# Kernel optimization log

Measured on AMD Instinct MI355X. Metric: run time of the kernel, lower is better.

The kernel has to match this reference:

```python
import jax, jax.numpy as jnp
import numpy as np

N = 50000      # nodes
E = 400000     # edges (before self-loops)
IN = 128       # in_channels
OUT = 64       # out_channels (per-head; concat=False averages heads)
HEADS = 8      # heads of first GAT layer; second layer has 1 head
NEG_SLOPE = 0.2


def _glorot(key, shape, fan_in, fan_out):
    s = jnp.sqrt(2.0 / (fan_in + fan_out)).astype(jnp.float32)
    return jax.random.normal(key, shape, jnp.float32) * s


def setup_inputs() -> dict:
    key = jax.random.key(0)
    ks = jax.random.split(key, 10)
    x = jax.random.normal(ks[0], (N, IN), jnp.float32)
    edge_index = jax.random.randint(ks[1], (2, E), 0, N)
    # layer 1: heads=HEADS, per-head dim OUT
    W1 = _glorot(ks[2], (IN, HEADS * OUT), IN, HEADS * OUT)
    att_src1 = _glorot(ks[3], (HEADS, OUT), OUT, 1)
    att_dst1 = _glorot(ks[4], (HEADS, OUT), OUT, 1)
    b1 = jnp.zeros((OUT,), jnp.float32)
    # layer 2: heads=1
    W2 = _glorot(ks[5], (OUT, 1 * OUT), OUT, OUT)
    att_src2 = _glorot(ks[6], (1, OUT), OUT, 1)
    att_dst2 = _glorot(ks[7], (1, OUT), OUT, 1)
    b2 = jnp.zeros((OUT,), jnp.float32)
    return dict(x=x, edge_index=edge_index, W1=W1, att_src1=att_src1,
                att_dst1=att_dst1, b1=b1, W2=W2, att_src2=att_src2,
                att_dst2=att_dst2, b2=b2)


def gat_conv(x, edge_index, W, att_src, att_dst, bias, heads, ch):
    """PyG GATConv with concat=False (mean over heads), add_self_loops=True."""
    n = x.shape[0]
    loop = jnp.arange(n, dtype=edge_index.dtype)
    src = jnp.concatenate([edge_index[0], loop])  # [E+N]
    dst = jnp.concatenate([edge_index[1], loop])
    h = (x @ W).reshape(n, heads, ch)                     # [N, H, C]
    a_s = jnp.sum(h * att_src, axis=-1)                   # [N, H]
    a_d = jnp.sum(h * att_dst, axis=-1)                   # [N, H]
    e = jax.nn.leaky_relu(a_s[src] + a_d[dst], NEG_SLOPE)  # [E+N, H]
    # numerically stable segment softmax over incoming edges of each dst node
    emax = jax.lax.stop_gradient(
        jax.ops.segment_max(e, dst, num_segments=n))       # [N, H]
    ee = jnp.exp(e - emax[dst])
    denom = jax.ops.segment_sum(ee, dst, num_segments=n)  # [N, H]
    alpha = ee / denom[dst]                                # [E+N, H]
    out = jax.ops.segment_sum(alpha[:, :, None] * h[src], dst,
                              num_segments=n)              # [N, H, C]
    return out.mean(axis=1) + bias                         # [N, C]


def reference(x, edge_index, W1, att_src1, att_dst1, b1,
              W2, att_src2, att_dst2, b2):
    h = gat_conv(x, edge_index, W1, att_src1, att_dst1, b1, HEADS, OUT)
    h = jax.nn.elu(h)
    return gat_conv(h, edge_index, W2, att_src2, att_dst2, b2, 1, OUT)
```

## Files before the change

### kernel.cpp

```cpp
#include <hip/hip_runtime.h>
#include <cstdint>
#include <cstddef>

#define NEG_SLOPE 0.2f

typedef short bf16x8 __attribute__((ext_vector_type(8)));
typedef float f32x4 __attribute__((ext_vector_type(4)));
typedef float f32x2 __attribute__((ext_vector_type(2)));

__device__ __forceinline__ unsigned short f2bf(float f) {
  unsigned u = __float_as_uint(f);
  u = u + 0x7FFFu + ((u >> 16) & 1u);
  return (unsigned short)(u >> 16);
}
__device__ __forceinline__ float bf2f(unsigned short b) {
  return __uint_as_float((unsigned)b << 16);
}
__device__ __forceinline__ f32x2 unpk(unsigned xv) {
  f32x2 r;
  r.x = __uint_as_float(xv << 16);
  r.y = __uint_as_float(xv & 0xFFFF0000u);
  return r;
}
__device__ __forceinline__ float rlf(float v, int l) {
  return __uint_as_float(
      (unsigned)__builtin_amdgcn_readlane((int)__float_as_uint(v), l));
}

__global__ __launch_bounds__(256) void prep_all(
    const int* __restrict__ ei, int* __restrict__ counts,
    const float* __restrict__ x, unsigned short* __restrict__ xb,
    const float* __restrict__ W1, const float* __restrict__ att_s1,
    const float* __restrict__ att_d1, unsigned short* __restrict__ AsAdT,
    unsigned short* __restrict__ WbT,
    const float* __restrict__ W2, unsigned short* __restrict__ W2t,
    const float* __restrict__ att_s2, const float* __restrict__ att_d2,
    float* __restrict__ AsAd2,
    int E, int ET, int N, int B0, int B1) {
  int b = blockIdx.x, tid = threadIdx.x;
  if (b < B0) {
    int i = b * 256 + tid;
    if (i < ET) {
      int dst = (i < E) ? ei[E + i] : (i - E);
      atomicAdd(&counts[dst], 1);
    }
    return;
  }
  b -= B0;
  if (b < B1) {
    int i = b * 256 + tid;
    if (i < N * 32) {
      float4 v = ((const float4*)x)[i];
      ushort4 o;
      o.x = f2bf(v.x); o.y = f2bf(v.y); o.z = f2bf(v.z); o.w = f2bf(v.w);
      ((ushort4*)xb)[i] = o;
    }
    return;
  }
  b -= B1;
  if (b < 8) {
    int i = b * 256 + tid;
    int o = i >> 7, k = i & 127, h = o & 7;
    const float* att = (o < 8) ? att_s1 : att_d1;
    float s = 0.f;
    for (int c = 0; c < 64; c++) s += W1[(size_t)k * 512 + h * 64 + c] * att[h * 64 + c];
    AsAdT[i] = f2bf(s);
    return;
  }
  b -= 8;
  if (b < 256) {
    int i = b * 256 + tid;
    int o = i >> 10, k = i & 1023, h = k >> 7, c = k & 127;
    WbT[i] = f2bf(W1[(size_t)c * 512 + h * 64 + o]);
    return;
  }
  b -= 256;
  if (b < 16) {
    int i = b * 256 + tid;
    if (i < 64 * 64) {
      int k = i >> 6, nn = i & 63;
      W2t[(size_t)nn * 64 + k] = f2bf(W2[i]);
    }
    return;
  }
  {
    int i = tid;
    if (i < 128) {
      int o = i >> 6, k = i & 63;
      const float* att = (o == 0) ? att_s2 : att_d2;
      float s = 0.f;
      for (int c = 0; c < 64; c++) s += W2[(size_t)k * 64 + c] * att[c];
      AsAd2[i] = s;
    }
  }
}

__global__ __launch_bounds__(1024) void scan_dots(
    const int* __restrict__ counts, int* __restrict__ offsets,
    const unsigned short* __restrict__ xb, const unsigned short* __restrict__ AsAdT,
    float* __restrict__ asd, int n) {
  if (blockIdx.x == 0) {
    __shared__ int sums[1024];
    int t = threadIdx.x;
    int chunk = (n + 1023) >> 10;
    int start = t * chunk;
    int end = min(start + chunk, n);
    int s = 0;
    for (int i = start; i < end; i++) s += counts[i];
    sums[t] = s;
    __syncthreads();
    for (int off = 1; off < 1024; off <<= 1) {
      int v = (t >= off) ? sums[t - off] : 0;
      __syncthreads();
      sums[t] += v;
      __syncthreads();
    }
    int run = sums[t] - s;
    for (int i = start; i < end; i++) { offsets[i] = run; run += counts[i]; }
    if (t == 1023) offsets[n] = sums[1023];
    return;
  }
  int tid = threadIdx.x;
  int wave = tid >> 6, lane = tid & 63;
  int q = lane >> 4, t = lane & 15;
  int row0 = (blockIdx.x - 1) * 256 + wave * 16;
  int arow = row0 + t; if (arow > n - 1) arow = n - 1;
  const bf16x8* aptr = (const bf16x8*)(xb + (size_t)arow * 128);
  const bf16x8* bptr = (const bf16x8*)(AsAdT + t * 128);
  f32x4 acc = (f32x4){0.f, 0.f, 0.f, 0.f};
  #pragma unroll
  for (int s = 0; s < 4; s++)
    acc = __builtin_amdgcn_mfma_f32_16x16x32_bf16(aptr[s * 4 + q], bptr[s * 4 + q],
                                                  acc, 0, 0, 0);
  #pragma unroll
  for (int r = 0; r < 4; r++) {
    int row = row0 + q * 4 + r;
    if (row < n) asd[row * 16 + t] = acc[r];
  }
}

__global__ __launch_bounds__(256) void fill_csr(
    const int* __restrict__ ei, const int* __restrict__ offsets,
    int* __restrict__ cursor, int* __restrict__ srcs, int E, int ET) {
  int i = blockIdx.x * 256 + threadIdx.x;
  if (i >= ET) return;
  int src, dst;
  if (i < E) { src = ei[i]; dst = ei[E + i]; } else { src = dst = i - E; }
  int pos = atomicAdd(&cursor[dst], 1);
  srcs[offsets[dst] + pos] = src;
}

#define CONSUME8R(RV, W, ACC)                                         \
  _Pragma("unroll")                                                   \
  for (int k = 0; k < 8; k++) {                                       \
    f32x2 x2 = unpk(RV[k]);                                           \
    ACC[0] += x2 * rlf(W, k * 8 + 0);                                 \
    ACC[1] += x2 * rlf(W, k * 8 + 1);                                 \
    ACC[2] += x2 * rlf(W, k * 8 + 2);                                 \
    ACC[3] += x2 * rlf(W, k * 8 + 3);                                 \
    ACC[4] += x2 * rlf(W, k * 8 + 4);                                 \
    ACC[5] += x2 * rlf(W, k * 8 + 5);                                 \
    ACC[6] += x2 * rlf(W, k * 8 + 6);                                 \
    ACC[7] += x2 * rlf(W, k * 8 + 7);                                 \
  }

__global__ __launch_bounds__(1024, 8) void agg1_gemm(
    const int* __restrict__ offsets, const int* __restrict__ srcs,
    const float* __restrict__ asd, const unsigned short* __restrict__ xb,
    const unsigned short* __restrict__ WbT, const float* __restrict__ b1,
    const float* __restrict__ AsAd2, unsigned short* __restrict__ zb,
    float* __restrict__ as2, float* __restrict__ ad2, int N) {
  __shared__ unsigned short sh[16 * 1032];
  int tid = threadIdx.x;
  int wv = tid >> 6, lane = tid & 63;
  int nb = blockIdx.x;
  {
    int node = nb * 16 + wv;
    f32x2 acc[8];
    #pragma unroll
    for (int h = 0; h < 8; h++) acc[h] = (f32x2){0.f, 0.f};
    float wsl = 0.f;
    int beg = offsets[node], end = offsets[node + 1];
    int jl = end - 1;
    float adv = asd[(size_t)node * 16 + 8 + (lane & 7)];
    for (int cb = beg; cb < end; cb += 16) {
      int cnt = min(16, end - cb);
      int sAll = srcs[min(cb + (lane & 15), jl)];
      int swa = srcs[min(cb + (lane >> 3), jl)];
      float asva = asd[(size_t)swa * 16 + (lane & 7)];
      float asvb = 0.f;
      if (cnt > 8) {
        int swb = srcs[min(cb + 8 + (lane >> 3), jl)];
        asvb = asd[(size_t)swb * 16 + (lane & 7)];
      }
      unsigned rva[8], rvb[8];
      #pragma unroll
      for (int k = 0; k < 8; k++) {
        int se = __builtin_amdgcn_readlane(sAll, k);
        rva[k] = *(const unsigned*)&xb[(size_t)(unsigned)se * 128 + 2 * lane];
      }
      if (cnt > 8) {
        #pragma unroll
        for (int k = 0; k < 8; k++) {
          int se = __builtin_amdgcn_readlane(sAll, k + 8);
          rvb[k] = *(const unsigned*)&xb[(size_t)(unsigned)se * 128 + 2 * lane];
        }
      }
      float wa, wb = 0.f;
      {
        float v = asva + adv;
        v = (v > 0.f) ? v : NEG_SLOPE * v;
        wa = (cb + (lane >> 3) < end) ? __expf(v) : 0.f;
      }
      if (cnt > 8) {
        float v = asvb + adv;
        v = (v > 0.f) ? v : NEG_SLOPE * v;
        wb = (cb + 8 + (lane >> 3) < end) ? __expf(v) : 0.f;
      }
      wsl += wa + wb;
      CONSUME8R(rva, wa, acc);
      if (cnt > 8) { CONSUME8R(rvb, wb, acc); }
    }
    wsl += __shfl_xor(wsl, 8, 64);
    wsl += __shfl_xor(wsl, 16, 64);
    wsl += __shfl_xor(wsl, 32, 64);
    #pragma unroll
    for (int h = 0; h < 8; h++) {
      float tot = rlf(wsl, h);
      float iv = 0.125f / tot;
      unsigned o = (unsigned)f2bf(acc[h].x * iv) | ((unsigned)f2bf(acc[h].y * iv) << 16);
      *(unsigned*)&sh[wv * 1032 + h * 128 + 2 * lane] = o;
    }
  }
  __syncthreads();
  if (wv < 4) {
    int q = lane >> 4, t = lane & 15;
    f32x4 acc4 = (f32x4){0.f, 0.f, 0.f, 0.f};
    const unsigned short* bbase = WbT + (size_t)(wv * 16 + t) * 1024;
    #pragma unroll 8
    for (int s = 0; s < 32; s++) {
      bf16x8 af = *(const bf16x8*)&sh[t * 1032 + s * 32 + q * 8];
      bf16x8 bf = *(const bf16x8*)&bbase[s * 32 + q * 8];
      acc4 = __builtin_amdgcn_mfma_f32_16x16x32_bf16(af, bf, acc4, 0, 0, 0);
    }
    int col = wv * 16 + t;
    float bias = b1[col];
    float vs = AsAd2[col], vd = AsAd2[64 + col];
    #pragma unroll
    for (int r = 0; r < 4; r++) {
      int row = q * 4 + r;
      int node = nb * 16 + row;
      float v = acc4[r] + bias;
      v = (v > 0.f) ? v : (__expf(v) - 1.f);
      zb[(size_t)node * 64 + col] = f2bf(v);
      float s = v * vs, d = v * vd;
      #pragma unroll
      for (int off = 1; off < 16; off <<= 1) {
        s += __shfl_xor(s, off, 64);
        d += __shfl_xor(d, off, 64);
      }
      if (t == 0) {
        atomicAdd(&as2[node], s);
        atomicAdd(&ad2[node], d);
      }
    }
  }
}

__global__ __launch_bounds__(1024, 8) void agg2_gemm(
    const int* __restrict__ offsets, const int* __restrict__ srcs,
    const float* __restrict__ as2, const float* __restrict__ ad2,
    const unsigned short* __restrict__ zb, const unsigned short* __restrict__ W2t,
    const float* __restrict__ b2, float* __restrict__ out, int N) {
  __shared__ unsigned short sh[16 * 72];
  int tid = threadIdx.x;
  int wv = tid >> 6, lane = tid & 63;
  int nb = blockIdx.x;
  {
    int node = nb * 16 + wv;
    int half = lane >> 5;
    float adv = ad2[node];
    int beg = offsets[node], end = offsets[node + 1];
    int jl = end - 1;
    f32x2 acc = (f32x2){0.f, 0.f};
    float wsl = 0.f;
    for (int cb = beg; cb < end; cb += 16) {
      int cnt = min(16, end - cb);
      int sAll = srcs[min(cb + (lane & 15), jl)];
      float asv = as2[sAll];
      unsigned rv[8];
      #pragma unroll
      for (int k = 0; k < 4; k++) {
        int s0 = __builtin_amdgcn_readlane(sAll, 2 * k);
        int s1 = __builtin_amdgcn_readlane(sAll, 2 * k + 1);
        int se = half ? s1 : s0;
        rv[k] = *(const unsigned*)&zb[(size_t)(unsigned)se * 64 + 2 * (lane & 31)];
      }
      if (cnt > 8) {
        #pragma unroll
        for (int k = 4; k < 8; k++) {
          int s0 = __builtin_amdgcn_readlane(sAll, 2 * k);
          int s1 = __builtin_amdgcn_readlane(sAll, 2 * k + 1);
          int se = half ? s1 : s0;
          rv[k] = *(const unsigned*)&zb[(size_t)(unsigned)se * 64 + 2 * (lane & 31)];
        }
      }
      float v = asv + adv;
      v = (v > 0.f) ? v : NEG_SLOPE * v;
      float wl = (cb + (lane & 15) < end) ? __expf(v) : 0.f;
      if (lane < 16) wsl += wl;
      #pragma unroll
      for (int k = 0; k < 4; k++) {
        float w0 = rlf(wl, 2 * k);
        float w1 = rlf(wl, 2 * k + 1);
        float w = half ? w1 : w0;
        acc += unpk(rv[k]) * w;
      }
      if (cnt > 8) {
        #pragma unroll
        for (int k = 4; k < 8; k++) {
          float w0 = rlf(wl, 2 * k);
          float w1 = rlf(wl, 2 * k + 1);
          float w = half ? w1 : w0;
          acc += unpk(rv[k]) * w;
        }
      }
    }
    wsl += __shfl_xor(wsl, 1, 64);
    wsl += __shfl_xor(wsl, 2, 64);
    wsl += __shfl_xor(wsl, 4, 64);
    wsl += __shfl_xor(wsl, 8, 64);
    float tot = rlf(wsl, 0);
    acc.x += __shfl_xor(acc.x, 32, 64);
    acc.y += __shfl_xor(acc.y, 32, 64);
    if (lane < 32) {
      float inv = 1.f / tot;
      unsigned o = (unsigned)f2bf(acc.x * inv) | ((unsigned)f2bf(acc.y * inv) << 16);
      *(unsigned*)&sh[wv * 72 + 2 * lane] = o;
    }
  }
  __syncthreads();
  if (wv < 4) {
    int q = lane >> 4, t = lane & 15;
    f32x4 acc4 = (f32x4){0.f, 0.f, 0.f, 0.f};
    const unsigned short* bbase = W2t + (size_t)(wv * 16 + t) * 64;
    #pragma unroll
    for (int s = 0; s < 2; s++) {
      bf16x8 af = *(const bf16x8*)&sh[t * 72 + s * 32 + q * 8];
      bf16x8 bf = *(const bf16x8*)&bbase[s * 32 + q * 8];
      acc4 = __builtin_amdgcn_mfma_f32_16x16x32_bf16(af, bf, acc4, 0, 0, 0);
    }
    int col = wv * 16 + t;
    float bias = b2[col];
    #pragma unroll
    for (int r = 0; r < 4; r++) {
      int node = nb * 16 + q * 4 + r;
      if (node < N) out[(size_t)node * 64 + col] = acc4[r] + bias;
    }
  }
}

extern "C" void kernel_launch(void* const* d_in, const int* in_sizes, int n_in,
                              void* d_out, int out_size, void* d_ws, size_t ws_size,
                              hipStream_t stream) {
  const int IN = 128;
  const int N = in_sizes[0] / IN;
  const int E = in_sizes[1] / 2;
  const int ET = E + N;

  const float* x        = (const float*)d_in[0];
  const int*   ei       = (const int*)d_in[1];
  const float* W1       = (const float*)d_in[2];
  const float* att_src1 = (const float*)d_in[3];
  const float* att_dst1 = (const float*)d_in[4];
  const float* b1       = (const float*)d_in[5];
  const float* W2       = (const float*)d_in[6];
  const float* att_src2 = (const float*)d_in[7];
  const float* att_dst2 = (const float*)d_in[8];
  const float* b2       = (const float*)d_in[9];
  float* out = (float*)d_out;

  char* base = (char*)d_ws;
  size_t off = 0;
  auto alloc = [&](size_t bytes) -> char* {
    char* p = base + off;
    off = (off + bytes + 255) & ~(size_t)255;
    return p;
  };
  unsigned short* xb    = (unsigned short*)alloc((size_t)N * 128 * 2);
  unsigned short* AsAdT = (unsigned short*)alloc((size_t)16 * 128 * 2);
  unsigned short* WbT   = (unsigned short*)alloc((size_t)64 * 1024 * 2);
  unsigned short* W2t   = (unsigned short*)alloc((size_t)64 * 64 * 2);
  unsigned short* zb    = (unsigned short*)alloc((size_t)N * 64 * 2);
  float* AsAd2 = (float*)alloc((size_t)128 * 4);
  float* asd1  = (float*)alloc((size_t)N * 16 * 4);
  int* offsets = (int*)alloc((size_t)(N + 1) * 4);
  int* srcs    = (int*)alloc((size_t)ET * 4);
  char* zero_begin = base + off;
  int* counts  = (int*)alloc((size_t)N * 4);
  int* cursor  = (int*)alloc((size_t)N * 4);
  float* a_s2  = (float*)alloc((size_t)N * 4);
  float* a_d2  = (float*)alloc((size_t)N * 4);
  char* zero_end = base + off;

  hipMemsetAsync(zero_begin, 0, (size_t)(zero_end - zero_begin), stream);

  const int TB = 256;
  auto cdiv = [](int a, int b) { return (a + b - 1) / b; };

  int B0 = cdiv(ET, TB);
  int B1 = cdiv(N * 32, TB);
  prep_all<<<B0 + B1 + 8 + 256 + 16 + 1, TB, 0, stream>>>(
      ei, counts, x, xb, W1, att_src1, att_dst1, AsAdT, WbT, W2, W2t,
      att_src2, att_dst2, AsAd2, E, ET, N, B0, B1);

  scan_dots<<<1 + cdiv(N, 256), 1024, 0, stream>>>(counts, offsets, xb, AsAdT,
                                                   asd1, N);

  fill_csr<<<cdiv(ET, TB), TB, 0, stream>>>(ei, offsets, cursor, srcs, E, ET);

  agg1_gemm<<<cdiv(N, 16), 1024, 0, stream>>>(offsets, srcs, asd1, xb, WbT, b1,
                                              AsAd2, zb, a_s2, a_d2, N);

  agg2_gemm<<<cdiv(N, 16), 1024, 0, stream>>>(offsets, srcs, a_s2, a_d2, zb,
                                              W2t, b2, out, N);
}
```

Baseline: 320.1 us.

## Use MFMA for layer-1 per-head weighted neighbor aggregation

Replaces the scalar FMA-with-readlane accumulation in agg1_gemm with 16x16x32 bf16 MFMA ops. Each chunk of 32 edges now builds an attention-weight A fragment (heads x edges) and B fragments of gathered bf16 features, repacked via shuffles. The attention weights are quantized to bf16 and the per-head sums are taken over those quantized values so the normalization stays consistent. Occupancy hint is reduced to 4 waves per SIMD to fit the larger f32x4 accumulators, and half the MFMA output rows (heads 8-15) are wasted, which adds padding cost in exchange for matrix-core throughput.

```diff
diff --git a/kernel.cpp b/kernel.cpp
--- a/kernel.cpp
+++ b/kernel.cpp
@@ -7,6 +7,7 @@
 typedef short bf16x8 __attribute__((ext_vector_type(8)));
 typedef float f32x4 __attribute__((ext_vector_type(4)));
 typedef float f32x2 __attribute__((ext_vector_type(2)));
+typedef unsigned u32x4 __attribute__((ext_vector_type(4)));
 
 __device__ __forceinline__ unsigned short f2bf(float f) {
   unsigned u = __float_as_uint(f);
@@ -150,21 +151,7 @@
   srcs[offsets[dst] + pos] = src;
 }
 
-#define CONSUME8R(RV, W, ACC)                                         \
-  _Pragma("unroll")                                                   \
-  for (int k = 0; k < 8; k++) {                                       \
-    f32x2 x2 = unpk(RV[k]);                                           \
-    ACC[0] += x2 * rlf(W, k * 8 + 0);                                 \
-    ACC[1] += x2 * rlf(W, k * 8 + 1);                                 \
-    ACC[2] += x2 * rlf(W, k * 8 + 2);                                 \
-    ACC[3] += x2 * rlf(W, k * 8 + 3);                                 \
-    ACC[4] += x2 * rlf(W, k * 8 + 4);                                 \
-    ACC[5] += x2 * rlf(W, k * 8 + 5);                                 \
-    ACC[6] += x2 * rlf(W, k * 8 + 6);                                 \
-    ACC[7] += x2 * rlf(W, k * 8 + 7);                                 \
-  }
-
-__global__ __launch_bounds__(1024, 8) void agg1_gemm(
+__global__ __launch_bounds__(1024, 4) void agg1_gemm(
     const int* __restrict__ offsets, const int* __restrict__ srcs,
     const float* __restrict__ asd, const unsigned short* __restrict__ xb,
     const unsigned short* __restrict__ WbT, const float* __restrict__ b1,
@@ -176,60 +163,82 @@
   int nb = blockIdx.x;
   {
     int node = nb * 16 + wv;
-    f32x2 acc[8];
+    int g = lane >> 4;
+    int h8 = lane & 7;
+    f32x4 acc[8];
     #pragma unroll
-    for (int h = 0; h < 8; h++) acc[h] = (f32x2){0.f, 0.f};
-    float wsl = 0.f;
+    for (int c = 0; c < 8; c++) acc[c] = (f32x4){0.f, 0.f, 0.f, 0.f};
+    float dsum = 0.f;
     int beg = offsets[node], end = offsets[node + 1];
     int jl = end - 1;
-    float adv = asd[(size_t)node * 16 + 8 + (lane & 7)];
-    for (int cb = beg; cb < end; cb += 16) {
-      int cnt = min(16, end - cb);
-      int sAll = srcs[min(cb + (lane & 15), jl)];
-      int swa = srcs[min(cb + (lane >> 3), jl)];
-      float asva = asd[(size_t)swa * 16 + (lane & 7)];
-      float asvb = 0.f;
-      if (cnt > 8) {
-        int swb = srcs[min(cb + 8 + (lane >> 3), jl)];
-        asvb = asd[(size_t)swb * 16 + (lane & 7)];
-      }
-      unsigned rva[8], rvb[8];
-      #pragma unroll
-      for (int k = 0; k < 8; k++) {
-        int se = __builtin_amdgcn_readlane(sAll, k);
-        rva[k] = *(const unsigned*)&xb[(size_t)(unsigned)se * 128 + 2 * lane];
-      }
-      if (cnt > 8) {
+    float adv = asd[(size_t)node * 16 + 8 + h8];
+    unsigned s = (lane & 1) * 16;
+    unsigned s2 = 16 - s;
+    unsigned msk = 0xFFFFu << s;
+    int choff = lane & 14;
+    for (int cb = beg; cb < end; cb += 32) {
+      int sAll = srcs[min(cb + (lane & 31), jl)];
+      float wj[8];
+      float dloc = 0.f;
+      #pragma unroll
+      for (int j = 0; j < 8; j++) {
+        int e = g * 8 + j;
+        int se = __shfl(sAll, e, 64);
+        float asv = asd[(size_t)(unsigned)se * 16 + h8];
+        float v = asv + adv;
+        v = (v > 0.f) ? v : NEG_SLOPE * v;
+        float w = (cb + e < end) ? __expf(v) : 0.f;
+        float wq = bf2f(f2bf(w));
+        wj[j] = wq;
+        dloc += wq;
+      }
+      dloc += __shfl_xor(dloc, 16, 64);
+      dloc += __shfl_xor(dloc, 32, 64);
+      dsum += dloc;
+      u32x4 a4;
+      #pragma unroll
+      for (int d = 0; d < 4; d++)
+        a4[d] = (unsigned)f2bf(wj[2 * d]) | ((unsigned)f2bf(wj[2 * d + 1]) << 16);
+      bf16x8 afr = __builtin_bit_cast(bf16x8, a4);
+      int seh[4];
+      #pragma unroll
+      for (int hh = 0; hh < 4; hh++)
+        seh[hh] = __shfl(sAll, g * 8 + hh * 2 + (lane & 1), 64);
+      unsigned own[8][4];
+      #pragma unroll
+      for (int cg = 0; cg < 8; cg++) {
         #pragma unroll
-        for (int k = 0; k < 8; k++) {
-          int se = __builtin_amdgcn_readlane(sAll, k + 8);
-          rvb[k] = *(const unsigned*)&xb[(size_t)(unsigned)se * 128 + 2 * lane];
+        for (int hh = 0; hh < 4; hh++)
+          own[cg][hh] = *(const unsigned*)&xb[(size_t)(unsigned)seh[hh] * 128 +
+                                              cg * 16 + choff];
+      }
+      #pragma unroll
+      for (int cg = 0; cg < 8; cg++) {
+        u32x4 b4;
+        #pragma unroll
+        for (int hh = 0; hh < 4; hh++) {
+          unsigned p = (unsigned)__shfl_xor((int)own[cg][hh], 1, 64);
+          b4[hh] = (own[cg][hh] & msk) | ((p >> s) << s2);
         }
-      }
-      float wa, wb = 0.f;
-      {
-        float v = asva + adv;
-        v = (v > 0.f) ? v : NEG_SLOPE * v;
-        wa = (cb + (lane >> 3) < end) ? __expf(v) : 0.f;
-      }
-      if (cnt > 8) {
-        float v = asvb + adv;
-        v = (v > 0.f) ? v : NEG_SLOPE * v;
-        wb = (cb + 8 + (lane >> 3) < end) ? __expf(v) : 0.f;
-      }
-      wsl += wa + wb;
-      CONSUME8R(rva, wa, acc);
-      if (cnt > 8) { CONSUME8R(rvb, wb, acc); }
-    }
-    wsl += __shfl_xor(wsl, 8, 64);
-    wsl += __shfl_xor(wsl, 16, 64);
-    wsl += __shfl_xor(wsl, 32, 64);
+        bf16x8 bfr = __builtin_bit_cast(bf16x8, b4);
+        acc[cg] = __builtin_amdgcn_mfma_f32_16x16x32_bf16(afr, bfr, acc[cg],
+                                                          0, 0, 0);
+      }
+    }
+    float scl = 0.125f / dsum;
+    float scl_r[4];
     #pragma unroll
-    for (int h = 0; h < 8; h++) {
-      float tot = rlf(wsl, h);
-      float iv = 0.125f / tot;
-      unsigned o = (unsigned)f2bf(acc[h].x * iv) | ((unsigned)f2bf(acc[h].y * iv) << 16);
-      *(unsigned*)&sh[wv * 1032 + h * 128 + 2 * lane] = o;
+    for (int r = 0; r < 4; r++)
+      scl_r[r] = __shfl(scl, (g * 4 + r) & 7, 64);
+    if (lane < 32) {
+      #pragma unroll
+      for (int cg = 0; cg < 8; cg++) {
+        #pragma unroll
+        for (int r = 0; r < 4; r++) {
+          float z = acc[cg][r] * scl_r[r];
+          sh[wv * 1032 + (g * 4 + r) * 128 + cg * 16 + (lane & 15)] = f2bf(z);
+        }
+      }
     }
   }
   __syncthreads();
```

Measured after the change: 380.0 us. +18.7%, slower.
